# Optimization experiments

Measured on AMD Instinct MI355X. Metric: run time of the kernel, lower is better.

Reference implementation:

```python
import jax, jax.numpy as jnp
import numpy as np

NUM_HEADS_Q = 32
NUM_HEADS_KV = 8
HEAD_DIM = 128
GROUPS = NUM_HEADS_Q // NUM_HEADS_KV


def rotate_half(x):
    d = x.shape[-1] // 2
    return jnp.concatenate([-x[..., d:], x[..., :d]], axis=-1)


def apply_rope(x, freq):
    # x: (b, h, s, d); freq: (1, 1, s, d) angles, broadcast over heads
    return x * jnp.cos(freq) + rotate_half(x) * jnp.sin(freq)


def setup_inputs() -> dict:
    key = jax.random.key(0)
    ks = jax.random.split(key, 6)
    b, s, d = 1, 2048, 4096
    x = jax.random.normal(ks[0], (b, s, d), dtype=jnp.float32)
    freq = jax.random.uniform(ks[1], (1, 1, s, HEAD_DIM), dtype=jnp.float32)
    sc = 1.0 / np.sqrt(d)
    wq = jax.random.normal(ks[2], (NUM_HEADS_Q * HEAD_DIM, d), dtype=jnp.float32) * sc
    wk = jax.random.normal(ks[3], (NUM_HEADS_KV * HEAD_DIM, d), dtype=jnp.float32) * sc
    wv = jax.random.normal(ks[4], (NUM_HEADS_KV * HEAD_DIM, d), dtype=jnp.float32) * sc
    wo = jax.random.normal(ks[5], (d, NUM_HEADS_Q * HEAD_DIM), dtype=jnp.float32) * sc
    return {"x": x, "freq": freq, "wq": wq, "wk": wk, "wv": wv, "wo": wo}


def reference(x, freq, wq, wk, wv, wo):
    b, s, d = x.shape
    # projections (nn.Linear: x @ W.T)
    q = (x @ wq.T).reshape(b, s, NUM_HEADS_Q, HEAD_DIM).transpose(0, 2, 1, 3)
    k = (x @ wk.T).reshape(b, s, NUM_HEADS_KV, HEAD_DIM).transpose(0, 2, 1, 3)
    v = (x @ wv.T).reshape(b, s, NUM_HEADS_KV, HEAD_DIM).transpose(0, 2, 1, 3)
    # past_kv is None -> seq_len offset 0
    q = apply_rope(q, freq)
    k = apply_rope(k, freq)
    k_new, v_new = k, v
    # repeat_interleave kv heads to match q heads (GQA)
    kr = jnp.repeat(k, GROUPS, axis=1)
    vr = jnp.repeat(v, GROUPS, axis=1)
    # scores: (b, hq, s, s)
    scores = jnp.einsum('bhqd,bhkd->bhqk', q, kr)
    causal = jnp.tril(jnp.ones((s, s), dtype=bool))
    scores = jnp.where(causal, scores, -jnp.inf)
    weights = jax.nn.softmax(scores * (HEAD_DIM ** -0.5), axis=-1)
    out = jnp.einsum('bhqk,bhkd->bhqd', weights, vr)
    out = out.transpose(0, 2, 1, 3).reshape(b, s, NUM_HEADS_Q * HEAD_DIM)
    return out @ wo.T, k_new, v_new
```

## Files before the change

kernel.cpp:

```cpp
#include <hip/hip_runtime.h>
#include <math.h>

#define S_LEN 2048
#define DMODEL 4096
#define NHQ 32
#define NHKV 8
#define HD 128
#define DQ 4096
#define DKV 1024
#define NQKV 6144

typedef __attribute__((ext_vector_type(8))) short bf16x8;
typedef __attribute__((ext_vector_type(4))) float f32x4;
typedef __attribute__((ext_vector_type(8))) unsigned short u16x8;

__device__ __forceinline__ unsigned short f2bf(float f) {
    unsigned u = __builtin_bit_cast(unsigned, f);
    u += 0x7fffu + ((u >> 16) & 1u);
    return (unsigned short)(u >> 16);
}

__device__ __forceinline__ void gload16(const void* g, void* l) {
    __builtin_amdgcn_global_load_lds(
        (const __attribute__((address_space(1))) unsigned int*)g,
        (__attribute__((address_space(3))) unsigned int*)l, 16, 0, 0);
}

__global__ __launch_bounds__(256) void cvt_bf16(const float* __restrict__ src,
                                                unsigned short* __restrict__ dst, int n8)
{
    for (int i = blockIdx.x * 256 + threadIdx.x; i < n8; i += gridDim.x * 256) {
        const float4 a = ((const float4*)src)[2 * i];
        const float4 b = ((const float4*)src)[2 * i + 1];
        u16x8 o;
        o[0] = f2bf(a.x); o[1] = f2bf(a.y); o[2] = f2bf(a.z); o[3] = f2bf(a.w);
        o[4] = f2bf(b.x); o[5] = f2bf(b.y); o[6] = f2bf(b.z); o[7] = f2bf(b.w);
        ((u16x8*)dst)[i] = o;
    }
}

#define BBM 128
#define BBN 128
#define BBK 32

__global__ __launch_bounds__(256) void gemm_bf16(const unsigned short* __restrict__ A,
                                                 const unsigned short* __restrict__ B,
                                                 float* __restrict__ C,
                                                 int M, int N, int K)
{
    __shared__ __align__(16) unsigned short As[BBM * BBK];
    __shared__ __align__(16) unsigned short Bs[BBN * BBK];

    const int tid  = threadIdx.x;
    const int lane = tid & 63;
    const int w    = tid >> 6;
    const int wy   = w >> 1, wx = w & 1;
    const int bm = blockIdx.y * BBM, bn = blockIdx.x * BBN;
    const int l15 = lane & 15;
    const int lk16 = (lane >> 4) * 16;
    const int ldsWaveBase = (tid & 192) * 16;

    f32x4 acc[4][4];
    #pragma unroll
    for (int m = 0; m < 4; ++m)
        #pragma unroll
        for (int n = 0; n < 4; ++n) acc[m][n] = (f32x4){0.f, 0.f, 0.f, 0.f};

    const char* Ab = (const char*)A;
    const char* Bb = (const char*)B;
    char* AsB = (char*)As;
    char* BsB = (char*)Bs;

    for (int k0 = 0; k0 < K; k0 += BBK) {
        __syncthreads();
        #pragma unroll
        for (int c = 0; c < 2; ++c) {
            const int i = tid + c * 256;
            const int r = i >> 2;
            const int co = (i & 3) << 4;
            gload16(Ab + ((size_t)(bm + r) * K + k0) * 2 + co, AsB + ldsWaveBase + c * 4096);
            gload16(Bb + ((size_t)(bn + r) * K + k0) * 2 + co, BsB + ldsWaveBase + c * 4096);
        }
        __syncthreads();

        bf16x8 af[4], bfr[4];
        #pragma unroll
        for (int m = 0; m < 4; ++m)
            af[m] = *(const bf16x8*)(AsB + (wy * 64 + m * 16 + l15) * 64 + lk16);
        #pragma unroll
        for (int n = 0; n < 4; ++n)
            bfr[n] = *(const bf16x8*)(BsB + (wx * 64 + n * 16 + l15) * 64 + lk16);
        #pragma unroll
        for (int m = 0; m < 4; ++m)
            #pragma unroll
            for (int n = 0; n < 4; ++n)
                acc[m][n] = __builtin_amdgcn_mfma_f32_16x16x32_bf16(af[m], bfr[n], acc[m][n], 0, 0, 0);
    }

    const int rg = (lane >> 4) * 4;
    #pragma unroll
    for (int m = 0; m < 4; ++m)
        #pragma unroll
        for (int n = 0; n < 4; ++n) {
            float* Cp = C + (size_t)(bm + wy * 64 + m * 16 + rg) * N + bn + wx * 64 + n * 16 + l15;
            #pragma unroll
            for (int r = 0; r < 4; ++r) Cp[(size_t)r * N] = acc[m][n][r];
        }
}

#define QSC (0.08838834764831845f * 1.4426950408889634f)

__global__ __launch_bounds__(256) void rope_q(const float* __restrict__ qkv,
                                              const float* __restrict__ freq,
                                              unsigned short* __restrict__ qbf)
{
    const int idx = blockIdx.x * 256 + threadIdx.x;
    const int d = idx & 63;
    const int s = (idx >> 6) & (S_LEN - 1);
    const int h = idx >> 17;
    const float f0 = freq[s * HD + d];
    const float f1 = freq[s * HD + d + 64];
    const float x0 = qkv[(size_t)s * NQKV + h * HD + d];
    const float x1 = qkv[(size_t)s * NQKV + h * HD + d + 64];
    const size_t ob = ((size_t)h * S_LEN + s) * HD + d;
    qbf[ob]      = f2bf((x0 * cosf(f0) - x1 * sinf(f0)) * QSC);
    qbf[ob + 64] = f2bf((x1 * cosf(f1) + x0 * sinf(f1)) * QSC);
}

__global__ __launch_bounds__(256) void rope_kv(const float* __restrict__ qkv,
                                               const float* __restrict__ freq,
                                               float* __restrict__ knew,
                                               float* __restrict__ vnew,
                                               unsigned short* __restrict__ kbf)
{
    const int idx = blockIdx.x * 256 + threadIdx.x;
    const int d = idx & 63;
    const int s = (idx >> 6) & (S_LEN - 1);
    const int h = idx >> 17;
    const float f0 = freq[s * HD + d];
    const float f1 = freq[s * HD + d + 64];
    const size_t ib = (size_t)s * NQKV + 4096 + h * HD + d;
    const float k0 = qkv[ib], k1 = qkv[ib + 64];
    const float v0 = qkv[ib + 1024], v1 = qkv[ib + 1024 + 64];
    const float k0r = k0 * cosf(f0) - k1 * sinf(f0);
    const float k1r = k1 * cosf(f1) + k0 * sinf(f1);
    const size_t ob = ((size_t)h * S_LEN + s) * HD + d;
    knew[ob] = k0r;       knew[ob + 64] = k1r;
    vnew[ob] = v0;        vnew[ob + 64] = v1;
    kbf[ob]  = f2bf(k0r); kbf[ob + 64]  = f2bf(k1r);
}

__global__ __launch_bounds__(256) void transp_v(const float* __restrict__ qkv,
                                                unsigned short* __restrict__ vT)
{
    __shared__ unsigned short T[64][72];
    const int s0 = blockIdx.x * 64;
    const int dt = blockIdx.y & 1;
    const int h  = blockIdx.y >> 1;
    const int d0 = dt * 64;
    const int tid = threadIdx.x;
    #pragma unroll
    for (int c = 0; c < 4; ++c) {
        const int i = tid + c * 256;
        const int r  = i >> 4;
        const int cc = (i & 15) * 4;
        const float4 v = *(const float4*)(qkv + (size_t)(s0 + r) * NQKV + 5120 + h * HD + d0 + cc);
        T[r][cc + 0] = f2bf(v.x); T[r][cc + 1] = f2bf(v.y);
        T[r][cc + 2] = f2bf(v.z); T[r][cc + 3] = f2bf(v.w);
    }
    __syncthreads();
    #pragma unroll
    for (int c = 0; c < 2; ++c) {
        const int i = tid + c * 256;
        const int dr = i >> 3;
        const int sc = (i & 7) * 8;
        u16x8 o;
        #pragma unroll
        for (int j = 0; j < 8; ++j) o[j] = T[sc + j][dr];
        *(u16x8*)(vT + ((size_t)(h * HD + d0 + dr)) * S_LEN + s0 + sc) = o;
    }
}

__global__ __launch_bounds__(256) void flash_bf16(const unsigned short* __restrict__ Qbf,
                                                  const unsigned short* __restrict__ Kbf,
                                                  const unsigned short* __restrict__ VbfT,
                                                  unsigned short* __restrict__ Obf)
{
    __shared__ __align__(16) unsigned short Ks[2][64 * 128];
    __shared__ __align__(16) unsigned short Vs[2][128 * 64];
    __shared__ __align__(16) unsigned short Ps[4][16 * 64];

    const int h  = blockIdx.x;
    const int yq = blockIdx.y;
    const int qt = (yq & 1) ? (31 - (yq >> 1)) : (yq >> 1);
    const int hkv = h >> 2;
    const int tid = threadIdx.x;
    const int lane = tid & 63;
    const int w = tid >> 6;
    const int l15 = lane & 15;
    const int l4  = lane >> 4;
    const int ldsWaveBase = (tid & 192) * 16;

    const char* Kg = (const char*)Kbf + (size_t)hkv * S_LEN * HD * 2;
    const char* Vg = (const char*)VbfT + (size_t)hkv * HD * S_LEN * 2;

    bf16x8 qf[4];
    {
        const char* Qg = (const char*)Qbf + ((size_t)h * S_LEN + qt * 64 + w * 16 + l15) * 256;
        #pragma unroll
        for (int kb = 0; kb < 4; ++kb)
            qf[kb] = *(const bf16x8*)(Qg + kb * 64 + l4 * 16);
    }

    auto STAGE = [&](int buf, int kt) {
        #pragma unroll
        for (int c = 0; c < 4; ++c) {
            const int i = tid + c * 256;
            const int kr = i >> 4;
            const int cc = (i & 15) ^ (kr & 7);
            gload16(Kg + (size_t)(kt * 64 + kr) * 256 + cc * 16,
                    (char*)Ks[buf] + ldsWaveBase + c * 4096);
        }
        #pragma unroll
        for (int c = 0; c < 4; ++c) {
            const int i = tid + c * 256;
            const int dr = i >> 3;
            const int cc = (i & 7) ^ (dr & 7);
            gload16(Vg + (size_t)dr * (S_LEN * 2) + (size_t)kt * 128 + cc * 16,
                    (char*)Vs[buf] + ldsWaveBase + c * 4096);
        }
    };

    f32x4 accO[8];
    #pragma unroll
    for (int n = 0; n < 8; ++n) accO[n] = (f32x4){0.f, 0.f, 0.f, 0.f};
    float m_i[4] = {-3e38f, -3e38f, -3e38f, -3e38f};
    float l_i[4] = {0.f, 0.f, 0.f, 0.f};

    STAGE(0, 0);
    __syncthreads();

    for (int kt = 0; kt <= qt; ++kt) {
        const int cbuf = kt & 1;
        if (kt < qt) STAGE(cbuf ^ 1, kt + 1);

        f32x4 sacc[4];
        #pragma unroll
        for (int n = 0; n < 4; ++n) sacc[n] = (f32x4){0.f, 0.f, 0.f, 0.f};
        __builtin_amdgcn_s_setprio(1);
        #pragma unroll
        for (int kb = 0; kb < 4; ++kb) {
            #pragma unroll
            for (int n = 0; n < 4; ++n) {
                const int krow = n * 16 + l15;
                const bf16x8 bk = *(const bf16x8*)((const char*)Ks[cbuf] + krow * 256 +
                                     ((kb * 64 + l4 * 16) ^ ((krow & 7) << 4)));
                sacc[n] = __builtin_amdgcn_mfma_f32_16x16x32_bf16(qf[kb], bk, sacc[n], 0, 0, 0);
            }
        }
        __builtin_amdgcn_s_setprio(0);

        float s0v[4], s1v[4], s2v[4], s3v[4], pm[4];
        #pragma unroll
        for (int reg = 0; reg < 4; ++reg) {
            float s0 = sacc[0][reg], s1 = sacc[1][reg];
            float s2 = sacc[2][reg], s3 = sacc[3][reg];
            if (kt == qt) {
                const int qglob = qt * 64 + w * 16 + l4 * 4 + reg;
                const int kvb = kt * 64 + l15;
                if (kvb +  0 > qglob) s0 = -3e38f;
                if (kvb + 16 > qglob) s1 = -3e38f;
                if (kvb + 32 > qglob) s2 = -3e38f;
                if (kvb + 48 > qglob) s3 = -3e38f;
            }
            float rmax = fmaxf(fmaxf(s0, s1), fmaxf(s2, s3));
            rmax = fmaxf(rmax, __shfl_xor(rmax, 1));
            rmax = fmaxf(rmax, __shfl_xor(rmax, 2));
            rmax = fmaxf(rmax, __shfl_xor(rmax, 4));
            rmax = fmaxf(rmax, __shfl_xor(rmax, 8));
            pm[reg] = rmax;
            s0v[reg] = s0; s1v[reg] = s1; s2v[reg] = s2; s3v[reg] = s3;
        }

        const bool grew = (pm[0] > m_i[0] + 8.f) || (pm[1] > m_i[1] + 8.f) ||
                          (pm[2] > m_i[2] + 8.f) || (pm[3] > m_i[3] + 8.f);
        if (__any(grew)) {
            #pragma unroll
            for (int reg = 0; reg < 4; ++reg) {
                const float mnew = fmaxf(m_i[reg], pm[reg]);
                const float csc = exp2f(m_i[reg] - mnew);
                l_i[reg] *= csc;
                m_i[reg] = mnew;
                #pragma unroll
                for (int n = 0; n < 8; ++n) accO[n][reg] *= csc;
            }
        }

        unsigned short* Pw = &Ps[w][0];
        #pragma unroll
        for (int reg = 0; reg < 4; ++reg) {
            const float p0 = exp2f(s0v[reg] - m_i[reg]);
            const float p1 = exp2f(s1v[reg] - m_i[reg]);
            const float p2 = exp2f(s2v[reg] - m_i[reg]);
            const float p3 = exp2f(s3v[reg] - m_i[reg]);
            const int rl = l4 * 4 + reg;
            const int sf = (rl & 7) << 4;
            *(unsigned short*)((char*)Pw + rl * 128 + (( 0 + l15 * 2) ^ sf)) = f2bf(p0);
            *(unsigned short*)((char*)Pw + rl * 128 + ((32 + l15 * 2) ^ sf)) = f2bf(p1);
            *(unsigned short*)((char*)Pw + rl * 128 + ((64 + l15 * 2) ^ sf)) = f2bf(p2);
            *(unsigned short*)((char*)Pw + rl * 128 + ((96 + l15 * 2) ^ sf)) = f2bf(p3);
            float rsum = p0 + p1 + p2 + p3;
            rsum += __shfl_xor(rsum, 1);
            rsum += __shfl_xor(rsum, 2);
            rsum += __shfl_xor(rsum, 4);
            rsum += __shfl_xor(rsum, 8);
            l_i[reg] += rsum;
        }

        const char* Pwb = (const char*)Pw;
        __builtin_amdgcn_s_setprio(1);
        #pragma unroll
        for (int kb = 0; kb < 2; ++kb) {
            const bf16x8 pa = *(const bf16x8*)(Pwb + l15 * 128 +
                                 ((kb * 64 + l4 * 16) ^ ((l15 & 7) << 4)));
            #pragma unroll
            for (int n = 0; n < 8; ++n) {
                const int vrow = n * 16 + l15;
                const bf16x8 vb = *(const bf16x8*)((const char*)Vs[cbuf] + vrow * 128 +
                                     ((kb * 64 + l4 * 16) ^ ((vrow & 7) << 4)));
                accO[n] = __builtin_amdgcn_mfma_f32_16x16x32_bf16(pa, vb, accO[n], 0, 0, 0);
            }
        }
        __builtin_amdgcn_s_setprio(0);

        __syncthreads();
    }

    float invl[4];
    #pragma unroll
    for (int reg = 0; reg < 4; ++reg) invl[reg] = 1.f / l_i[reg];
    #pragma unroll
    for (int n = 0; n < 8; ++n)
        #pragma unroll
        for (int reg = 0; reg < 4; ++reg) {
            const int row = qt * 64 + w * 16 + l4 * 4 + reg;
            Obf[(size_t)row * DQ + h * HD + n * 16 + l15] = f2bf(accO[n][reg] * invl[reg]);
        }
}

extern "C" void kernel_launch(void* const* d_in, const int* in_sizes, int n_in,
                              void* d_out, int out_size, void* d_ws, size_t ws_size,
                              hipStream_t stream)
{
    const float* x    = (const float*)d_in[0];
    const float* freq = (const float*)d_in[1];
    const float* wq   = (const float*)d_in[2];
    const float* wk   = (const float*)d_in[3];
    const float* wv   = (const float*)d_in[4];
    const float* wo   = (const float*)d_in[5];

    float* out  = (float*)d_out;
    float* knew = out + (size_t)S_LEN * DQ;
    float* vnew = knew + (size_t)NHKV * S_LEN * HD;

    char* ws = (char*)d_ws;
    unsigned short* x_bf    = (unsigned short*)(ws);
    unsigned short* attn_bf = (unsigned short*)(ws);
    unsigned short* wqkv_bf = (unsigned short*)(ws + (16u << 20));
    unsigned short* wo_bf   = (unsigned short*)(ws + (16u << 20));
    float*          qkv_f32 = (float*)(ws + (64u << 20));
    unsigned short* q_bf    = (unsigned short*)(ws + (112u << 20));
    unsigned short* k_bf    = (unsigned short*)(ws + (128u << 20));
    unsigned short* vT_bf   = (unsigned short*)(ws + (132u << 20));

    const dim3 blk(256);

    cvt_bf16<<<2048, blk, 0, stream>>>(x,  x_bf, S_LEN * DMODEL / 8);
    cvt_bf16<<<2048, blk, 0, stream>>>(wq, wqkv_bf, DQ * DMODEL / 8);
    cvt_bf16<<<1024, blk, 0, stream>>>(wk, wqkv_bf + (size_t)DQ * DMODEL, DKV * DMODEL / 8);
    cvt_bf16<<<1024, blk, 0, stream>>>(wv, wqkv_bf + (size_t)(DQ + DKV) * DMODEL, DKV * DMODEL / 8);

    gemm_bf16<<<dim3(NQKV / BBN, S_LEN / BBM), blk, 0, stream>>>(x_bf, wqkv_bf, qkv_f32, S_LEN, NQKV, DMODEL);

    cvt_bf16<<<2048, blk, 0, stream>>>(wo, wo_bf, DMODEL * DQ / 8);

    rope_q<<<NHQ * S_LEN * 64 / 256, blk, 0, stream>>>(qkv_f32, freq, q_bf);
    rope_kv<<<NHKV * S_LEN * 64 / 256, blk, 0, stream>>>(qkv_f32, freq, knew, vnew, k_bf);
    transp_v<<<dim3(S_LEN / 64, 2 * NHKV), blk, 0, stream>>>(qkv_f32, vT_bf);

    flash_bf16<<<dim3(NHQ, S_LEN / 64), blk, 0, stream>>>(q_bf, k_bf, vT_bf, attn_bf);

    gemm_bf16<<<dim3(DMODEL / BBN, S_LEN / BBM), blk, 0, stream>>>(attn_bf, wo_bf, out, S_LEN, DMODEL, DMODEL);
}
```

Measured before the change: 589.4 us.

## Multi-buffer GEMM LDS tiles with async prefetch pipeline and XCD-aware block remap

Rewrites the bf16 GEMM main loop to use a 4-slot LDS ring buffer, prefetching tiles three iterations ahead with global_load_lds. Explicit vmcnt/lgkmcnt waits and barriers replace the two __syncthreads per iteration, so global loads overlap MFMA work. Block IDs are remapped so consecutive tiles land on the same XCD for better L2 reuse, and setprio raises wave priority around the MFMA block. LDS use grows fourfold, which may lower occupancy, and the hand-counted vmcnt values must match the number of outstanding loads.

```diff
diff --git a/kernel.cpp b/kernel.cpp
--- a/kernel.cpp
+++ b/kernel.cpp
@@ -48,14 +48,20 @@
                                                  float* __restrict__ C,
                                                  int M, int N, int K)
 {
-    __shared__ __align__(16) unsigned short As[BBM * BBK];
-    __shared__ __align__(16) unsigned short Bs[BBN * BBK];
+    __shared__ __align__(16) unsigned short As[4][BBM * BBK];
+    __shared__ __align__(16) unsigned short Bs[4][BBN * BBK];
 
     const int tid  = threadIdx.x;
     const int lane = tid & 63;
     const int w    = tid >> 6;
     const int wy   = w >> 1, wx = w & 1;
-    const int bm = blockIdx.y * BBM, bn = blockIdx.x * BBN;
+
+    const int gX  = gridDim.x;
+    const int nwg = gX * gridDim.y;
+    int id = blockIdx.y * gX + blockIdx.x;
+    id = (id & 7) * (nwg >> 3) + (id >> 3);
+    const int bm = (id / gX) * BBM, bn = (id % gX) * BBN;
+
     const int l15 = lane & 15;
     const int lk16 = (lane >> 4) * 16;
     const int ldsWaveBase = (tid & 192) * 16;
@@ -68,33 +74,57 @@
 
     const char* Ab = (const char*)A;
     const char* Bb = (const char*)B;
-    char* AsB = (char*)As;
-    char* BsB = (char*)Bs;
-
-    for (int k0 = 0; k0 < K; k0 += BBK) {
-        __syncthreads();
+    const int NT = K / BBK;
+
+    auto STAGE = [&](int slot, int t) {
         #pragma unroll
         for (int c = 0; c < 2; ++c) {
             const int i = tid + c * 256;
             const int r = i >> 2;
             const int co = (i & 3) << 4;
-            gload16(Ab + ((size_t)(bm + r) * K + k0) * 2 + co, AsB + ldsWaveBase + c * 4096);
-            gload16(Bb + ((size_t)(bn + r) * K + k0) * 2 + co, BsB + ldsWaveBase + c * 4096);
-        }
-        __syncthreads();
-
+            gload16(Ab + ((size_t)(bm + r) * K + t * BBK) * 2 + co,
+                    (char*)As + slot * 8192 + ldsWaveBase + c * 4096);
+            gload16(Bb + ((size_t)(bn + r) * K + t * BBK) * 2 + co,
+                    (char*)Bs + slot * 8192 + ldsWaveBase + c * 4096);
+        }
+    };
+
+    STAGE(0, 0); STAGE(1, 1); STAGE(2, 2);
+
+    for (int t = 0; t < NT; ++t) {
+        __builtin_amdgcn_sched_barrier(0);
+        asm volatile("s_waitcnt lgkmcnt(0)" ::: "memory");
+        __builtin_amdgcn_s_barrier();
+        __builtin_amdgcn_sched_barrier(0);
+
+        const int ts = t + 3;
+        if (ts < NT) STAGE(ts & 3, ts);
+
+        const int rem = NT - 1 - t;
+        if (rem >= 3)      asm volatile("s_waitcnt vmcnt(12)" ::: "memory");
+        else if (rem == 2) asm volatile("s_waitcnt vmcnt(8)"  ::: "memory");
+        else if (rem == 1) asm volatile("s_waitcnt vmcnt(4)"  ::: "memory");
+        else               asm volatile("s_waitcnt vmcnt(0)"  ::: "memory");
+        __builtin_amdgcn_sched_barrier(0);
+        __builtin_amdgcn_s_barrier();
+        __builtin_amdgcn_sched_barrier(0);
+
+        const char* Asl = (const char*)As + (t & 3) * 8192;
+        const char* Bsl = (const char*)Bs + (t & 3) * 8192;
         bf16x8 af[4], bfr[4];
         #pragma unroll
         for (int m = 0; m < 4; ++m)
-            af[m] = *(const bf16x8*)(AsB + (wy * 64 + m * 16 + l15) * 64 + lk16);
+            af[m] = *(const bf16x8*)(Asl + (wy * 64 + m * 16 + l15) * 64 + lk16);
         #pragma unroll
         for (int n = 0; n < 4; ++n)
-            bfr[n] = *(const bf16x8*)(BsB + (wx * 64 + n * 16 + l15) * 64 + lk16);
+            bfr[n] = *(const bf16x8*)(Bsl + (wx * 64 + n * 16 + l15) * 64 + lk16);
+        __builtin_amdgcn_s_setprio(1);
         #pragma unroll
         for (int m = 0; m < 4; ++m)
             #pragma unroll
             for (int n = 0; n < 4; ++n)
                 acc[m][n] = __builtin_amdgcn_mfma_f32_16x16x32_bf16(af[m], bfr[n], acc[m][n], 0, 0, 0);
+        __builtin_amdgcn_s_setprio(0);
     }
 
     const int rg = (lane >> 4) * 4;
```

New measurement: 613.3 us. +4.0%, slower.

## Use 256x256 double-buffered MFMA GEMM for fused QKV projection

Applied to the files above, without the earlier changes.

Adds a new bf16 GEMM kernel with 256x256 block tiles, 512 threads, BK=64 and double-buffered LDS filled through global_load_lds. Loads for the next k-tile are issued in quarters and interleaved with MFMA compute, and LDS reads use XOR swizzling. The kernel replaces the 128x128 GEMM for the QKV projection to raise data reuse per block and overlap memory with compute. In exchange it uses 128KB of LDS per block and launches only 24x8 blocks, which may leave some compute units underused.

```diff
diff --git a/kernel.cpp b/kernel.cpp
--- a/kernel.cpp
+++ b/kernel.cpp
@@ -37,6 +37,123 @@
         o[4] = f2bf(b.x); o[5] = f2bf(b.y); o[6] = f2bf(b.z); o[7] = f2bf(b.w);
         ((u16x8*)dst)[i] = o;
     }
+}
+
+#define GBM 256
+#define GBN 256
+
+__global__ __launch_bounds__(512, 2) void gemm_bf16_256(const unsigned short* __restrict__ A,
+                                                        const unsigned short* __restrict__ B,
+                                                        float* __restrict__ C,
+                                                        int M, int N, int K)
+{
+    __shared__ __align__(16) unsigned short As[2][256 * 64];
+    __shared__ __align__(16) unsigned short Bs[2][256 * 64];
+
+    const int tid  = threadIdx.x;
+    const int lane = tid & 63;
+    const int w    = tid >> 6;
+    const int wy   = w >> 2, wx = w & 3;
+    const int bm = blockIdx.y * GBM, bn = blockIdx.x * GBN;
+    const int l15 = lane & 15, l4 = lane >> 4;
+    const int lr  = lane >> 3;
+    const int lc  = ((lane & 7) * 16) ^ (lane & 32);
+    const int swzR = (l15 & 4) << 3;
+
+    f32x4 acc[8][4];
+    #pragma unroll
+    for (int m = 0; m < 8; ++m)
+        #pragma unroll
+        for (int n = 0; n < 4; ++n) acc[m][n] = (f32x4){0.f, 0.f, 0.f, 0.f};
+
+    const char* Ab = (const char*)A;
+    const char* Bb = (const char*)B;
+    const int NT = K / 64;
+
+    auto STAGE = [&](int nb, int kt, int sl) {
+        #pragma unroll
+        for (int j = 0; j < 2; ++j) {
+            const int rsb = w * 8 + j * 64;
+            if (sl == 0 || sl == 3) {
+                const int mh = (sl == 3);
+                const int rb = (rsb & 63) + mh * 64 + ((rsb & 64) ? 128 : 0);
+                gload16(Ab + ((size_t)(bm + rb + lr) * K + kt * 64) * 2 + lc,
+                        (char*)As + nb * 32768 + rb * 128);
+            } else {
+                const int nh = (sl == 2);
+                const int rb = (rsb >> 5) * 64 + nh * 32 + (rsb & 31);
+                gload16(Bb + ((size_t)(bn + rb + lr) * K + kt * 64) * 2 + lc,
+                        (char*)Bs + nb * 32768 + rb * 128);
+            }
+        }
+    };
+
+    STAGE(0, 0, 0); STAGE(0, 0, 1); STAGE(0, 0, 2); STAGE(0, 0, 3);
+
+    bf16x8 af[4][2], bfr[2][2];
+
+    for (int t = 0; t < NT; ++t) {
+        const int cb = t & 1, nb = cb ^ 1;
+        const char* Ac = (const char*)As + cb * 32768;
+        const char* Bc = (const char*)Bs + cb * 32768;
+        const bool last = (t == NT - 1);
+
+        #pragma unroll
+        for (int p = 0; p < 4; ++p) {
+            const int mh = p >> 1, nh = p & 1;
+
+            if (!last) {
+                STAGE(nb, t + 1, p);
+                asm volatile("s_waitcnt vmcnt(6)" ::: "memory");
+            } else {
+                if (p == 0)      asm volatile("s_waitcnt vmcnt(4)" ::: "memory");
+                else if (p == 1) asm volatile("s_waitcnt vmcnt(2)" ::: "memory");
+                else             asm volatile("s_waitcnt vmcnt(0)" ::: "memory");
+            }
+            __builtin_amdgcn_sched_barrier(0);
+            __builtin_amdgcn_s_barrier();
+            __builtin_amdgcn_sched_barrier(0);
+
+            if (nh == 0) {
+                #pragma unroll
+                for (int mm = 0; mm < 4; ++mm)
+                    #pragma unroll
+                    for (int ks = 0; ks < 2; ++ks)
+                        af[mm][ks] = *(const bf16x8*)(Ac +
+                            (wy * 128 + (mh * 4 + mm) * 16 + l15) * 128 +
+                            ((ks * 64 + l4 * 16) ^ swzR));
+            }
+            #pragma unroll
+            for (int nn = 0; nn < 2; ++nn)
+                #pragma unroll
+                for (int ks = 0; ks < 2; ++ks)
+                    bfr[nn][ks] = *(const bf16x8*)(Bc +
+                        (wx * 64 + (nh * 2 + nn) * 16 + l15) * 128 +
+                        ((ks * 64 + l4 * 16) ^ swzR));
+
+            __builtin_amdgcn_s_setprio(1);
+            #pragma unroll
+            for (int ks = 0; ks < 2; ++ks)
+                #pragma unroll
+                for (int mm = 0; mm < 4; ++mm)
+                    #pragma unroll
+                    for (int nn = 0; nn < 2; ++nn)
+                        acc[mh * 4 + mm][nh * 2 + nn] =
+                            __builtin_amdgcn_mfma_f32_16x16x32_bf16(
+                                af[mm][ks], bfr[nn][ks], acc[mh * 4 + mm][nh * 2 + nn], 0, 0, 0);
+            __builtin_amdgcn_s_setprio(0);
+        }
+    }
+
+    const int rg = l4 * 4;
+    #pragma unroll
+    for (int m = 0; m < 8; ++m)
+        #pragma unroll
+        for (int n = 0; n < 4; ++n) {
+            float* Cp = C + (size_t)(bm + wy * 128 + m * 16 + rg) * N + bn + wx * 64 + n * 16 + l15;
+            #pragma unroll
+            for (int r = 0; r < 4; ++r) Cp[(size_t)r * N] = acc[m][n][r];
+        }
 }
 
 #define BBM 128
@@ -380,7 +497,8 @@
     cvt_bf16<<<1024, blk, 0, stream>>>(wk, wqkv_bf + (size_t)DQ * DMODEL, DKV * DMODEL / 8);
     cvt_bf16<<<1024, blk, 0, stream>>>(wv, wqkv_bf + (size_t)(DQ + DKV) * DMODEL, DKV * DMODEL / 8);
 
-    gemm_bf16<<<dim3(NQKV / BBN, S_LEN / BBM), blk, 0, stream>>>(x_bf, wqkv_bf, qkv_f32, S_LEN, NQKV, DMODEL);
+    gemm_bf16_256<<<dim3(NQKV / GBN, S_LEN / GBM), dim3(512), 0, stream>>>(
+        x_bf, wqkv_bf, qkv_f32, S_LEN, NQKV, DMODEL);
 
     cvt_bf16<<<2048, blk, 0, stream>>>(wo, wo_bf, DMODEL * DQ / 8);
 
```

New measurement: 589.5 us. About the same (+0.0%).
